# Optimization experiments

Measured on AMD Instinct MI355X. Metric: run time of the kernel, lower is better.

## Reference

```python
import jax, jax.numpy as jnp
import numpy as np


def setup_inputs() -> dict:
    key = jax.random.key(0)
    k1, k2, k3 = jax.random.split(key, 3)
    # NCHW input, OIHW weight (matches torch CustomConv)
    x = jax.random.normal(k1, (32, 128, 56, 56), dtype=jnp.float32)
    weight = jax.random.uniform(k2, (256, 128, 3, 3), dtype=jnp.float32)
    bias = jax.random.uniform(k3, (256,), dtype=jnp.float32)
    return {"x": x, "weight": weight, "bias": bias}


def reference(x, weight, bias):
    # The original CUDA path is unfold (im2col) -> matmul (appx_mode=0 => exact)
    # -> bias add -> reshape to (B, oC, H, W). That is exactly conv2d + bias.
    # stride=(1,1), padding=(1,1), dilation=(1,1) per init_kwargs.
    out = jax.lax.conv_general_dilated(
        x, weight,
        window_strides=(1, 1),
        padding=((1, 1), (1, 1)),
        rhs_dilation=(1, 1),
        dimension_numbers=("NCHW", "OIHW", "NCHW"),
    )
    return out + bias[None, :, None, None]
```

## Files before the change

kernel.cpp:

```cpp
#include <hip/hip_runtime.h>
#include <hip/hip_bf16.h>
#include <stdint.h>


#define CB    32
#define CIC   128
#define CH    56
#define CW    56
#define COC   256
#define CK    1152
#define PLANES (CB*CIC)
#define PH    58
#define PW    64
#define PLANE_SZ (PH*PW)
#define QV    (CH*PW)
#define KB_STEPS (CK/64)
#define WT_SLAB (COC*64)

typedef short     bf16x8  __attribute__((ext_vector_type(8)));
typedef float     f32x4   __attribute__((ext_vector_type(4)));
typedef unsigned short u16x8 __attribute__((ext_vector_type(8)));

__global__ __launch_bounds__(256)
void pad_x_kernel(const float* __restrict__ x, ushort* __restrict__ xp, int total4) {
    int t = blockIdx.x * 256 + threadIdx.x;
    if (t >= total4) return;
    int i4 = t * 4;
    int plane = i4 / PLANE_SZ;
    int rem   = i4 - plane * PLANE_SZ;
    int r = rem / PW;
    int c0 = rem - r * PW;
    ushort4 v;
    ushort* pv = (ushort*)&v;
#pragma unroll
    for (int j = 0; j < 4; ++j) {
        int c = c0 + j;
        float val = 0.f;
        if (plane < PLANES && r >= 1 && r <= CH && c >= 1 && c <= CW) {
            val = x[((size_t)plane * CH + (r - 1)) * CW + (c - 1)];
        }
        __hip_bfloat16 b = __float2bfloat16(val);
        pv[j] = *(ushort*)&b;
    }
    *(ushort4*)(xp + i4) = v;
}

__global__ __launch_bounds__(256)
void repack_wt_kernel(const float* __restrict__ w, ushort* __restrict__ wt) {
    int t = blockIdx.x * 256 + threadIdx.x;
    if (t >= COC * CK) return;
    int oc = t / CK;
    int k  = t - oc * CK;
    int kb = k >> 6, kl = k & 63;
    int pos = kb * WT_SLAB + (((oc << 6) + kl) ^ ((oc & 7) << 3));
    __hip_bfloat16 b = __float2bfloat16(w[t]);
    wt[pos] = *(ushort*)&b;
}

__device__ __forceinline__ void gload_lds16(const void* g, void* l) {
    __builtin_amdgcn_global_load_lds(
        (const __attribute__((address_space(1))) uint32_t*)g,
        (__attribute__((address_space(3))) uint32_t*)l, 16, 0, 0);
}

__global__ __launch_bounds__(256, 2)
void conv_mfma_kernel(const ushort* __restrict__ wt, const ushort* __restrict__ xp,
                      const float* __restrict__ bias, float* __restrict__ out) {
    __shared__ ushort ldsA[128 * 64];
    __shared__ ushort ldsB[128 * 64];

    const int tid  = threadIdx.x;
    const int lane = tid & 63;
    const int wid  = tid >> 6;
    const int wm   = wid >> 1, wn = wid & 1;
    const int n_img = blockIdx.x / 28;
    const int q0    = (blockIdx.x % 28) * 128;
    const int oc0   = blockIdx.y * 128;

    const int qq = tid & 31;
    const int ko = tid >> 5;

    f32x4 acc[4][4];
#pragma unroll
    for (int m = 0; m < 4; ++m)
#pragma unroll
        for (int n = 0; n < 4; ++n)
#pragma unroll
            for (int e = 0; e < 4; ++e) acc[m][n][e] = 0.f;

    const size_t plane_base = (size_t)n_img * CIC * PLANE_SZ;

    for (int kb = 0; kb < KB_STEPS; ++kb) {
        uint32_t bq[8][2];
#pragma unroll
        for (int r = 0; r < 8; ++r) {
            int k  = kb * 64 + ko * 8 + r;
            int ic = k / 9;
            int t9 = k - ic * 9;
            int kh = t9 / 3;
            int kw = t9 - kh * 3;
            size_t e = plane_base + (size_t)ic * PLANE_SZ + kh * PW + kw + q0 + 4 * qq;
            size_t a0 = e & ~(size_t)3;
            int s = (int)(e & 3);
            uint2 d01 = *(const uint2*)(xp + a0);
            uint32_t d2 = *(const uint32_t*)(xp + a0 + 4);
            uint64_t v01 = ((uint64_t)d01.y << 32) | d01.x;
            uint64_t v12 = ((uint64_t)d2    << 32) | d01.y;
            bq[r][0] = (uint32_t)(v01 >> (16 * s));
            bq[r][1] = (uint32_t)(v12 >> (16 * s));
        }

        __syncthreads();

        {
            const char* src = (const char*)(wt + (size_t)kb * WT_SLAB + oc0 * 64);
            char* dstbase = (char*)ldsA;
#pragma unroll
            for (int c = 0; c < 4; ++c) {
                int chunk = (wid * 4 + c) * 1024;
                gload_lds16(src + chunk + lane * 16, dstbase + chunk);
            }
        }

#pragma unroll
        for (int i = 0; i < 4; ++i) {
            int q = 4 * qq + i;
            u16x8 v;
#pragma unroll
            for (int r = 0; r < 8; ++r) {
                uint32_t srcw = (i < 2) ? bq[r][0] : bq[r][1];
                v[r] = (unsigned short)(srcw >> (16 * (i & 1)));
            }
            uint32_t bo = (uint32_t)(q * 128 + ko * 16) ^ (uint32_t)(((q >> 2) & 7) << 4);
            *(u16x8*)((char*)ldsB + bo) = v;
        }

        __syncthreads();

#pragma unroll
        for (int kk = 0; kk < 2; ++kk) {
            bf16x8 af[4], bfr[4];
#pragma unroll
            for (int m = 0; m < 4; ++m) {
                int oc_l = wm * 64 + m * 16 + (lane & 15);
                uint32_t bo = (uint32_t)(oc_l * 128 + kk * 64 + (lane >> 4) * 16)
                              ^ (uint32_t)((oc_l & 7) << 4);
                af[m] = *(const bf16x8*)((const char*)ldsA + bo);
            }
#pragma unroll
            for (int n = 0; n < 4; ++n) {
                int q_l = wn * 64 + n * 16 + (lane & 15);
                uint32_t bo = (uint32_t)(q_l * 128 + kk * 64 + (lane >> 4) * 16)
                              ^ (uint32_t)(((q_l >> 2) & 7) << 4);
                bfr[n] = *(const bf16x8*)((const char*)ldsB + bo);
            }
#pragma unroll
            for (int m = 0; m < 4; ++m)
#pragma unroll
                for (int n = 0; n < 4; ++n)
                    acc[m][n] = __builtin_amdgcn_mfma_f32_16x16x32_bf16(af[m], bfr[n], acc[m][n], 0, 0, 0);
        }
    }

#pragma unroll
    for (int m = 0; m < 4; ++m) {
        float bv[4];
        int oc_b = oc0 + wm * 64 + m * 16 + (lane >> 4) * 4;
#pragma unroll
        for (int r = 0; r < 4; ++r) bv[r] = bias[oc_b + r];
#pragma unroll
        for (int n = 0; n < 4; ++n) {
            int q_virt = q0 + wn * 64 + n * 16 + (lane & 15);
            int wcol = q_virt & 63;
            if (wcol >= CW) continue;
            int h = q_virt >> 6;
#pragma unroll
            for (int r = 0; r < 4; ++r) {
                int oc = oc_b + r;
                out[(((size_t)n_img * COC + oc) * CH + h) * CW + wcol] = acc[m][n][r] + bv[r];
            }
        }
    }
}

__global__ __launch_bounds__(256)
void conv3x3_fallback(const float* __restrict__ x, const float* __restrict__ w,
                      const float* __restrict__ bias, float* __restrict__ out) {
    const int ow  = threadIdx.x & 63;
    const int ocg = threadIdx.x >> 6;
    const int oh  = blockIdx.y;
    const int n   = blockIdx.z;
    if (ow >= CW) return;
    const int oc0 = blockIdx.x * 32 + ocg * 8;
    float acc[8];
#pragma unroll
    for (int j = 0; j < 8; ++j) acc[j] = 0.f;
    const float* xn = x + (size_t)n * CIC * CH * CW;
    for (int ic = 0; ic < CIC; ++ic) {
        const float* xc = xn + (size_t)ic * CH * CW;
#pragma unroll
        for (int kh = 0; kh < 3; ++kh) {
            const int ih = oh + kh - 1;
            if ((unsigned)ih >= (unsigned)CH) continue;
            const float* xr = xc + ih * CW;
            const float xm = (ow > 0)      ? xr[ow - 1] : 0.f;
            const float x0 =                 xr[ow];
            const float xp_ = (ow < CW - 1) ? xr[ow + 1] : 0.f;
#pragma unroll
            for (int j = 0; j < 8; ++j) {
                const float* wj = w + (size_t)(oc0 + j) * CK + ic * 9 + kh * 3;
                acc[j] = fmaf(wj[0], xm, acc[j]);
                acc[j] = fmaf(wj[1], x0, acc[j]);
                acc[j] = fmaf(wj[2], xp_, acc[j]);
            }
        }
    }
    const size_t obase = (((size_t)n * COC + oc0) * CH + oh) * CW + ow;
#pragma unroll
    for (int j = 0; j < 8; ++j)
        out[obase + (size_t)j * CH * CW] = acc[j] + bias[oc0 + j];
}

extern "C" void kernel_launch(void* const* d_in, const int* in_sizes, int n_in,
                              void* d_out, int out_size, void* d_ws, size_t ws_size,
                              hipStream_t stream) {
    const float* x    = (const float*)d_in[0];
    const float* w    = (const float*)d_in[1];
    const float* bias = (const float*)d_in[2];
    float* out        = (float*)d_out;

    const size_t wt_bytes  = (size_t)KB_STEPS * WT_SLAB * sizeof(ushort);
    const size_t xp_off    = 1u << 20;
    const int    xp_elems  = PLANES * PLANE_SZ + 512;
    const size_t need      = xp_off + (size_t)xp_elems * sizeof(ushort);

    if (ws_size < need) {
        dim3 grid(COC / 32, CH, CB);
        conv3x3_fallback<<<grid, 256, 0, stream>>>(x, w, bias, out);
        return;
    }

    ushort* wt = (ushort*)d_ws;
    ushort* xp = (ushort*)((char*)d_ws + xp_off);

    const int total4 = xp_elems / 4;
    pad_x_kernel<<<(total4 + 255) / 256, 256, 0, stream>>>(x, xp, total4);
    repack_wt_kernel<<<(COC * CK + 255) / 256, 256, 0, stream>>>(w, wt);

    dim3 grid(28 * CB, 2);
    conv_mfma_kernel<<<grid, 256, 0, stream>>>(wt, xp, bias, out);
}
```

Measured before the change: 153.1 us.

## Reorder K by kw and add pre-shifted input copies for aligned loads

Reorders the reduction dimension so kw is outermost, and builds two extra copies of the padded bf16 input shifted by one and two elements. The GEMM kernel can then fetch B operands with single aligned 8-byte loads instead of unaligned load-and-shift sequences. Per-thread offsets are now updated incrementally instead of recomputing div/mod every step, and the LDS swizzle addresses are precomputed. In exchange it adds an extra pass that writes two more copies of the input, and uses three times the workspace, falling back to the old path when the workspace is too small.

```diff
diff --git a/kernel.cpp b/kernel.cpp
--- a/kernel.cpp
+++ b/kernel.cpp
@@ -13,9 +13,13 @@
 #define PH    58
 #define PW    64
 #define PLANE_SZ (PH*PW)
-#define QV    (CH*PW)
 #define KB_STEPS (CK/64)
 #define WT_SLAB (COC*64)
+#define XS_ELEMS (PLANES*PLANE_SZ+512)
+#define XS_STRIDE XS_ELEMS
+#define NPLANE_D 475136
+#define DEL_A 78016
+#define DEL_B 3520
 
 typedef short     bf16x8  __attribute__((ext_vector_type(8)));
 typedef float     f32x4   __attribute__((ext_vector_type(4)));
@@ -28,8 +32,8 @@
     int i4 = t * 4;
     int plane = i4 / PLANE_SZ;
     int rem   = i4 - plane * PLANE_SZ;
-    int r = rem / PW;
-    int c0 = rem - r * PW;
+    int r = rem >> 6;
+    int c0 = rem & 63;
     ushort4 v;
     ushort* pv = (ushort*)&v;
 #pragma unroll
@@ -46,14 +50,37 @@
 }
 
 __global__ __launch_bounds__(256)
+void shift2_kernel(const ushort* __restrict__ xs0, ushort* __restrict__ xs1,
+                   ushort* __restrict__ xs2, int total8) {
+    int t = blockIdx.x * 256 + threadIdx.x;
+    if (t >= total8) return;
+    int i8 = t * 8;
+    uint4 a = *(const uint4*)(xs0 + i8);
+    uint32_t b = *(const uint32_t*)(xs0 + i8 + 8);
+    uint4 c1, c2;
+    c1.x = (uint32_t)((((uint64_t)a.y << 32) | a.x) >> 16);
+    c1.y = (uint32_t)((((uint64_t)a.z << 32) | a.y) >> 16);
+    c1.z = (uint32_t)((((uint64_t)a.w << 32) | a.z) >> 16);
+    c1.w = (uint32_t)((((uint64_t)b   << 32) | a.w) >> 16);
+    c2.x = a.y; c2.y = a.z; c2.z = a.w; c2.w = b;
+    *(uint4*)(xs1 + i8) = c1;
+    *(uint4*)(xs2 + i8) = c2;
+}
+
+__global__ __launch_bounds__(256)
 void repack_wt_kernel(const float* __restrict__ w, ushort* __restrict__ wt) {
     int t = blockIdx.x * 256 + threadIdx.x;
     if (t >= COC * CK) return;
     int oc = t / CK;
-    int k  = t - oc * CK;
-    int kb = k >> 6, kl = k & 63;
-    int pos = kb * WT_SLAB + (((oc << 6) + kl) ^ ((oc & 7) << 3));
-    __hip_bfloat16 b = __float2bfloat16(w[t]);
+    int k2 = t - oc * CK;
+    int kw  = k2 / 384;
+    int rem = k2 - kw * 384;
+    int ic  = rem / 3;
+    int kh  = rem - ic * 3;
+    int korig = ic * 9 + kh * 3 + kw;
+    int kb = k2 >> 6, kl = k2 & 63;
+    int pos = kb * WT_SLAB + (oc << 6) + (kl ^ ((oc & 7) << 3));
+    __hip_bfloat16 b = __float2bfloat16(w[(size_t)oc * CK + korig]);
     wt[pos] = *(ushort*)&b;
 }
 
@@ -63,8 +90,9 @@
         (__attribute__((address_space(3))) uint32_t*)l, 16, 0, 0);
 }
 
+template <int MODE>
 __global__ __launch_bounds__(256, 2)
-void conv_mfma_kernel(const ushort* __restrict__ wt, const ushort* __restrict__ xp,
+void conv_mfma_kernel(const ushort* __restrict__ wt, const ushort* __restrict__ xs,
                       const float* __restrict__ bias, float* __restrict__ out) {
     __shared__ ushort ldsA[128 * 64];
     __shared__ ushort ldsB[128 * 64];
@@ -77,8 +105,8 @@
     const int q0    = (blockIdx.x % 28) * 128;
     const int oc0   = blockIdx.y * 128;
 
-    const int qq = tid & 31;
-    const int ko = tid >> 5;
+    const int ko = tid & 7;
+    const int qq = tid >> 3;
 
     f32x4 acc[4][4];
 #pragma unroll
@@ -88,26 +116,61 @@
 #pragma unroll
             for (int e = 0; e < 4; ++e) acc[m][n][e] = 0.f;
 
-    const size_t plane_base = (size_t)n_img * CIC * PLANE_SZ;
+    int off[8], khs[8];
+    int i3 = ko * 8;
+    {
+        const int nbase = n_img * NPLANE_D + q0 + 4 * qq;
+#pragma unroll
+        for (int r = 0; r < 8; ++r) {
+            int kp = ko * 8 + r;
+            int ic = kp / 3;
+            int kh = kp - ic * 3;
+            off[r] = nbase + ic * PLANE_SZ + kh * PW;
+            khs[r] = kh;
+        }
+    }
+
+    uint32_t wbyte[4];
+#pragma unroll
+    for (int i = 0; i < 4; ++i) {
+        int q = 4 * qq + i;
+        wbyte[i] = (uint32_t)(q * 128 + ((ko ^ (q & 7)) << 4));
+    }
+    uint32_t fr_off[2];
+#pragma unroll
+    for (int kk = 0; kk < 2; ++kk) {
+        int octet = kk * 4 + (lane >> 4);
+        fr_off[kk] = (uint32_t)((octet ^ (lane & 7)) << 4);
+    }
+    const uint32_t abase = (uint32_t)((wm * 64 + (lane & 15)) * 128);
+    const uint32_t bbase = (uint32_t)((wn * 64 + (lane & 15)) * 128);
 
     for (int kb = 0; kb < KB_STEPS; ++kb) {
-        uint32_t bq[8][2];
+        uint2 bqd[8];
+        if (MODE == 0) {
+#pragma unroll
+            for (int r = 0; r < 8; ++r)
+                bqd[r] = *(const uint2*)(xs + off[r]);
+        } else {
+#pragma unroll
+            for (int r = 0; r < 8; ++r) {
+                int a0 = off[r] & ~3;
+                int s  = off[r] & 3;
+                uint2 d01 = *(const uint2*)(xs + a0);
+                uint32_t d2 = *(const uint32_t*)(xs + a0 + 4);
+                bqd[r].x = (uint32_t)(((((uint64_t)d01.y) << 32) | d01.x) >> (16 * s));
+                bqd[r].y = (uint32_t)(((((uint64_t)d2)    << 32) | d01.y) >> (16 * s));
+            }
+        }
+
+        const bool cross = (i3 + 64 >= 384);
+        i3 = cross ? (i3 + 64 - 384) : (i3 + 64);
 #pragma unroll
         for (int r = 0; r < 8; ++r) {
-            int k  = kb * 64 + ko * 8 + r;
-            int ic = k / 9;
-            int t9 = k - ic * 9;
-            int kh = t9 / 3;
-            int kw = t9 - kh * 3;
-            size_t e = plane_base + (size_t)ic * PLANE_SZ + kh * PW + kw + q0 + 4 * qq;
-            size_t a0 = e & ~(size_t)3;
-            int s = (int)(e & 3);
-            uint2 d01 = *(const uint2*)(xp + a0);
-            uint32_t d2 = *(const uint32_t*)(xp + a0 + 4);
-            uint64_t v01 = ((uint64_t)d01.y << 32) | d01.x;
-            uint64_t v12 = ((uint64_t)d2    << 32) | d01.y;
-            bq[r][0] = (uint32_t)(v01 >> (16 * s));
-            bq[r][1] = (uint32_t)(v12 >> (16 * s));
+            bool khw = (khs[r] == 2);
+            khs[r] = khw ? 0 : (khs[r] + 1);
+            off[r] += DEL_A + (khw ? DEL_B : 0);
+            if (cross) off[r] += (MODE == 0 ? (XS_STRIDE - NPLANE_D) : (1 - NPLANE_D));
         }
 
         __syncthreads();
@@ -124,15 +187,13 @@
 
 #pragma unroll
         for (int i = 0; i < 4; ++i) {
-            int q = 4 * qq + i;
-            u16x8 v;
+            u16x8 vv;
 #pragma unroll
             for (int r = 0; r < 8; ++r) {
-                uint32_t srcw = (i < 2) ? bq[r][0] : bq[r][1];
-                v[r] = (unsigned short)(srcw >> (16 * (i & 1)));
-            }
-            uint32_t bo = (uint32_t)(q * 128 + ko * 16) ^ (uint32_t)(((q >> 2) & 7) << 4);
-            *(u16x8*)((char*)ldsB + bo) = v;
+                uint32_t w32 = (i < 2) ? bqd[r].x : bqd[r].y;
+                vv[r] = (unsigned short)(w32 >> (16 * (i & 1)));
+            }
+            *(u16x8*)((char*)ldsB + wbyte[i]) = vv;
         }
 
         __syncthreads();
@@ -141,19 +202,11 @@
         for (int kk = 0; kk < 2; ++kk) {
             bf16x8 af[4], bfr[4];
 #pragma unroll
-            for (int m = 0; m < 4; ++m) {
-                int oc_l = wm * 64 + m * 16 + (lane & 15);
-                uint32_t bo = (uint32_t)(oc_l * 128 + kk * 64 + (lane >> 4) * 16)
-                              ^ (uint32_t)((oc_l & 7) << 4);
-                af[m] = *(const bf16x8*)((const char*)ldsA + bo);
-            }
-#pragma unroll
-            for (int n = 0; n < 4; ++n) {
-                int q_l = wn * 64 + n * 16 + (lane & 15);
-                uint32_t bo = (uint32_t)(q_l * 128 + kk * 64 + (lane >> 4) * 16)
-                              ^ (uint32_t)(((q_l >> 2) & 7) << 4);
-                bfr[n] = *(const bf16x8*)((const char*)ldsB + bo);
-            }
+            for (int m = 0; m < 4; ++m)
+                af[m] = *(const bf16x8*)((const char*)ldsA + (abase + m * 2048 + fr_off[kk]));
+#pragma unroll
+            for (int n = 0; n < 4; ++n)
+                bfr[n] = *(const bf16x8*)((const char*)ldsB + (bbase + n * 2048 + fr_off[kk]));
 #pragma unroll
             for (int m = 0; m < 4; ++m)
 #pragma unroll
@@ -229,24 +282,32 @@
     const float* bias = (const float*)d_in[2];
     float* out        = (float*)d_out;
 
-    const size_t wt_bytes  = (size_t)KB_STEPS * WT_SLAB * sizeof(ushort);
-    const size_t xp_off    = 1u << 20;
-    const int    xp_elems  = PLANES * PLANE_SZ + 512;
-    const size_t need      = xp_off + (size_t)xp_elems * sizeof(ushort);
-
-    if (ws_size < need) {
+    const size_t xs_off   = 1u << 20;
+    const size_t xs_bytes = (size_t)XS_ELEMS * sizeof(ushort);
+    const size_t need1    = xs_off + xs_bytes;
+    const size_t need3    = xs_off + 3 * xs_bytes;
+
+    if (ws_size < need1) {
         dim3 grid(COC / 32, CH, CB);
         conv3x3_fallback<<<grid, 256, 0, stream>>>(x, w, bias, out);
         return;
     }
 
-    ushort* wt = (ushort*)d_ws;
-    ushort* xp = (ushort*)((char*)d_ws + xp_off);
-
-    const int total4 = xp_elems / 4;
-    pad_x_kernel<<<(total4 + 255) / 256, 256, 0, stream>>>(x, xp, total4);
+    ushort* wt  = (ushort*)d_ws;
+    ushort* xs0 = (ushort*)((char*)d_ws + xs_off);
+
+    const int total4 = XS_ELEMS / 4;
+    pad_x_kernel<<<(total4 + 255) / 256, 256, 0, stream>>>(x, xs0, total4);
     repack_wt_kernel<<<(COC * CK + 255) / 256, 256, 0, stream>>>(w, wt);
 
     dim3 grid(28 * CB, 2);
-    conv_mfma_kernel<<<grid, 256, 0, stream>>>(wt, xp, bias, out);
-}
+    if (ws_size >= need3) {
+        ushort* xs1 = xs0 + XS_STRIDE;
+        ushort* xs2 = xs1 + XS_STRIDE;
+        const int total8 = XS_ELEMS / 8;
+        shift2_kernel<<<(total8 + 255) / 256, 256, 0, stream>>>(xs0, xs1, xs2, total8);
+        conv_mfma_kernel<0><<<grid, 256, 0, stream>>>(wt, xs0, bias, out);
+    } else {
+        conv_mfma_kernel<1><<<grid, 256, 0, stream>>>(wt, xs0, bias, out);
+    }
+}
```

Result: slower. 237.9 us (+55.4%).
